# Kernel optimization log

Measured on AMD Instinct MI355X. Metric: run time of the kernel, lower is better.

Reference implementation:

```python
import jax, jax.numpy as jnp
import numpy as np

B, T, D, H = 32, 1024, 1024, 1024


def gru_cell(x, h, W_ih, W_hh, b_ih, b_hh):
    # torch.nn.GRUCell math; gate order (r, z, n)
    gi = x @ W_ih.T + b_ih          # [B, 3H]
    gh = h @ W_hh.T + b_hh          # [B, 3H]
    i_r, i_z, i_n = jnp.split(gi, 3, axis=-1)
    h_r, h_z, h_n = jnp.split(gh, 3, axis=-1)
    r = jax.nn.sigmoid(i_r + h_r)
    z = jax.nn.sigmoid(i_z + h_z)
    n = jnp.tanh(i_n + r * h_n)
    return (1.0 - z) * n + z * h


def setup_inputs() -> dict:
    key = jax.random.key(0)
    k = jax.random.split(key, 6)
    scale = np.float32(1.0 / np.sqrt(H))  # torch GRUCell init range
    x = jax.random.normal(k[0], (B, T, D), jnp.float32)
    seg = jax.random.randint(k[1], (B, T), 0, 2).astype(jnp.int32)
    W_ih = jax.random.normal(k[2], (3 * H, D), jnp.float32) * scale
    W_hh = jax.random.normal(k[3], (3 * H, H), jnp.float32) * scale
    b_ih = jax.random.normal(k[4], (3 * H,), jnp.float32) * scale
    b_hh = jax.random.normal(k[5], (3 * H,), jnp.float32) * scale
    return {"x": x, "W_ih": W_ih, "W_hh": W_hh, "b_ih": b_ih, "b_hh": b_hh, "seg": seg}


def reference(x, W_ih, W_hh, b_ih, b_hh, seg):
    # apply_rnn_pack: GRUCell scan with segment-masked reset + ragged pack.
    segf = seg.astype(x.dtype)

    def step(h, inp):
        xt, st = inp                      # xt [B,D], st [B]
        h_new = gru_cell(xt, h, W_ih, W_hh, b_ih, b_hh)
        h_next = st[:, None] * h_new      # reset hidden where seg==0
        return h_next, h_new              # emit pre-reset hidden

    h0 = jnp.zeros((B, H), x.dtype)
    xs = (jnp.swapaxes(x, 0, 1), jnp.swapaxes(segf, 0, 1))
    _, hs = jax.lax.scan(step, h0, xs)    # hs [T,B,H]
    hs = jnp.swapaxes(hs, 0, 1)           # [B,T,H]

    # Pack: write h at step t into slot (#emits before t) iff seg[b,t]==0.
    emit = seg == 0                       # [B,T]
    pos = jnp.cumsum(emit, axis=1) - 1    # destination slot for emitted steps
    pos = jnp.where(emit, pos, T)         # route non-emitted steps to pad slot
    out = jnp.zeros((B, T + 1, H), x.dtype)
    b_idx = jnp.arange(B)[:, None]
    out = out.at[b_idx, pos].set(hs)
    out = out[:, :T]                      # [B,T,H], ragged-padded with zeros
    counts = emit.sum(axis=1)             # per-sample packed lengths (idx)
    return out, counts
```

## Files before the change

kernel.cpp:

```cpp
#include <hip/hip_runtime.h>

#define NB 32
#define NT 1024
#define ND 1024
#define NH 1024
#define G3 3072
#define MROWS 32768
#define HROWS 16512
#define GSROWS 32896
#define TAILG 128

typedef __bf16 bf16x8 __attribute__((ext_vector_type(8)));
typedef float f32x4 __attribute__((ext_vector_type(4)));
typedef unsigned short u16x8 __attribute__((ext_vector_type(8)));
typedef unsigned short u16x4 __attribute__((ext_vector_type(4)));

__device__ __forceinline__ float b2f(unsigned short u){
  union { unsigned int i; float f; } v; v.i = ((unsigned int)u) << 16; return v.f;
}
__device__ __forceinline__ unsigned short f2b(float f){
  union { float f; unsigned int i; } v; v.f = f;
  unsigned int r = (v.i + 0x7FFFu + ((v.i >> 16) & 1u)) >> 16;
  return (unsigned short)r;
}
__device__ __forceinline__ float sigm(float x){ return 1.0f / (1.0f + __expf(-x)); }
__device__ __forceinline__ float tanh_(float x){ return 2.0f / (1.0f + __expf(-2.0f * x)) - 1.0f; }

__device__ __forceinline__ void g2l16(const void* g, void* l){
  __builtin_amdgcn_global_load_lds((__attribute__((address_space(1))) void*)g,
                                   (__attribute__((address_space(3))) void*)l, 16, 0, 0);
}

__global__ __launch_bounds__(256) void k_setup(const float* __restrict__ wih,
    const float* __restrict__ whh, const float* __restrict__ x,
    unsigned short* __restrict__ wih_b, unsigned short* __restrict__ whh_b,
    unsigned short* __restrict__ x_b, int has_xb, f32x4* __restrict__ outv, int out_n4){
  int i0 = blockIdx.x * 256 + threadIdx.x;
  int stride = gridDim.x * 256;
  f32x4 z = {0.f, 0.f, 0.f, 0.f};
  for (int j = i0; j < out_n4; j += stride) __builtin_nontemporal_store(z, &outv[j]);
  int nw4 = (G3 * ND) / 4;
  for (int j = i0; j < nw4; j += stride){
    f32x4 a = ((const f32x4*)wih)[j];
    f32x4 b = ((const f32x4*)whh)[j];
    u16x4 ua = {f2b(a[0]), f2b(a[1]), f2b(a[2]), f2b(a[3])};
    u16x4 ub = {f2b(b[0]), f2b(b[1]), f2b(b[2]), f2b(b[3])};
    ((u16x4*)wih_b)[j] = ua;
    ((u16x4*)whh_b)[j] = ub;
  }
  if (has_xb){
    int nx4 = (MROWS * ND) / 4;
    for (int j = i0; j < nx4; j += stride){
      f32x4 a = ((const f32x4*)x)[j];
      u16x4 u = {f2b(a[0]), f2b(a[1]), f2b(a[2]), f2b(a[3])};
      ((u16x4*)x_b)[j] = u;
    }
  }
}

__global__ __launch_bounds__(1024) void k_segbuild(const int* __restrict__ seg,
    int* __restrict__ ugi, int* __restrict__ uout, int* __restrict__ ulen,
    int* __restrict__ nseg_b,
    int* __restrict__ sgi, int* __restrict__ sout, int* __restrict__ slen,
    int* __restrict__ cnt_ge, int* __restrict__ base_g,
    unsigned int* __restrict__ perm, unsigned int* __restrict__ bar,
    float* __restrict__ counts_out){
  __shared__ int hist[1025];
  __shared__ int sufx[1024];
  __shared__ int pref[1024];
  __shared__ int offs[1025];
  int tid = threadIdx.x;
  int wave = tid >> 6, lane = tid & 63;
  if (tid == 0) *bar = 0u;

  for (int b = wave; b < NB; b += 16){
    int prev = -1;
    int zc = 0;
    for (int c = 0; c < 16; ++c){
      int t = c * 64 + lane;
      int v = seg[b * NT + t];
      unsigned long long mask = __ballot(v == 0);
      unsigned long long below = mask & ((1ULL << lane) - 1ULL);
      if (v == 0){
        int pz = below ? (c * 64 + (63 - __clzll((long long)below))) : prev;
        int eidx = zc + __popcll(below);
        int slot = b * NT + eidx;
        ugi[slot]  = b * NT + (pz + 1);
        uout[slot] = b * NT + eidx;
        ulen[slot] = t - pz;
      }
      if (mask) prev = c * 64 + (63 - __clzll((long long)mask));
      zc += __popcll(mask);
    }
    if (lane == 0){ nseg_b[b] = zc; counts_out[b] = (float)zc; }
  }
  __syncthreads();
  for (int i = tid; i <= 1024; i += 1024) hist[i] = 0;
  __syncthreads();
  for (int s = tid; s < NB * NT; s += 1024){
    int b = s >> 10, j = s & 1023;
    if (j < nseg_b[b]) atomicAdd(&hist[ulen[s]], 1);
  }
  __syncthreads();
  if (tid < 1024) sufx[tid] = hist[tid + 1];
  __syncthreads();
  for (int off = 1; off < 1024; off <<= 1){
    int v = (tid + off < 1024) ? sufx[tid + off] : 0;
    __syncthreads();
    sufx[tid] += v;
    __syncthreads();
  }
  cnt_ge[tid + 1] = sufx[tid];
  if (tid == 0){ cnt_ge[0] = sufx[0]; cnt_ge[1025] = 0; }
  offs[tid] = sufx[tid];
  if (tid == 0) offs[1024] = 0;
  pref[tid] = sufx[tid];
  __syncthreads();
  for (int off = 1; off < 1024; off <<= 1){
    int v = (tid >= off) ? pref[tid - off] : 0;
    __syncthreads();
    pref[tid] += v;
    __syncthreads();
  }
  base_g[tid + 1] = pref[tid];
  if (tid == 0){ base_g[0] = 0; base_g[1025] = pref[1023]; }
  __syncthreads();
  for (int s = tid; s < NB * NT; s += 1024){
    int b = s >> 10, j = s & 1023;
    if (j < nseg_b[b]){
      int len = ulen[s];
      int p = atomicAdd(&offs[len], 1);
      sgi[p] = ugi[s]; sout[p] = uout[s]; slen[p] = len;
    }
  }
  for (int m = tid; m < MROWS; m += 1024) perm[m] = 0xFFFFFFFFu;
  __syncthreads();
  int nseg = cnt_ge[1];
  for (int p = tid; p < nseg; p += 1024){
    int src = sgi[p];
    int len = slen[p];
    perm[src] = (unsigned int)p;
    for (int kk = 1; kk < len; ++kk)
      perm[src + kk] = (unsigned int)(pref[kk - 1] + p);
  }
}

__global__ __launch_bounds__(256, 2) void k_gi_gemm(const float* __restrict__ x,
    const unsigned short* __restrict__ x_b, const unsigned short* __restrict__ wih_b,
    const float* __restrict__ b_ih, const unsigned int* __restrict__ perm,
    unsigned short* __restrict__ gs, int use_xb){
  __shared__ unsigned short Alds[128 * 64];
  __shared__ unsigned short Blds[128 * 64];
  int tid = threadIdx.x;
  int w = tid >> 6, lane = tid & 63;
  int mtile = blockIdx.x / 24, ntile = blockIdx.x % 24;
  int m0 = mtile * 128, n0 = ntile * 128;
  int mh = (w >> 1) * 64, nh = (w & 1) * 64;
  int lrow = lane >> 3;
  int lcol = 8 * ((lane & 7) ^ lrow);
  f32x4 acc[4][4];
#pragma unroll
  for (int i = 0; i < 4; ++i)
#pragma unroll
    for (int j = 0; j < 4; ++j) acc[i][j] = (f32x4){0.f, 0.f, 0.f, 0.f};

  for (int kc = 0; kc < 16; ++kc){
    __syncthreads();
    if (use_xb){
#pragma unroll
      for (int p = 0; p < 4; ++p){
        int s = w * 4 + p;
        g2l16(x_b + (size_t)(m0 + s * 8 + lrow) * ND + kc * 64 + lcol, &Alds[s * 512]);
      }
    } else {
#pragma unroll
      for (int p = 0; p < 4; ++p){
        int e = (p * 256 + tid) * 8;
        int r = e >> 6, c = e & 63;
        const float* src = x + (size_t)(m0 + r) * ND + kc * 64 + c;
        f32x4 f0 = *(const f32x4*)src;
        f32x4 f1 = *(const f32x4*)(src + 4);
        u16x8 u;
        u[0]=f2b(f0[0]); u[1]=f2b(f0[1]); u[2]=f2b(f0[2]); u[3]=f2b(f0[3]);
        u[4]=f2b(f1[0]); u[5]=f2b(f1[1]); u[6]=f2b(f1[2]); u[7]=f2b(f1[3]);
        *(u16x8*)&Alds[r * 64 + (c ^ ((r & 7) << 3))] = u;
      }
    }
#pragma unroll
    for (int p = 0; p < 4; ++p){
      int s = w * 4 + p;
      g2l16(wih_b + (size_t)(n0 + s * 8 + lrow) * ND + kc * 64 + lcol, &Blds[s * 512]);
    }
    __syncthreads();
#pragma unroll
    for (int ks = 0; ks < 2; ++ks){
      int co = ks * 32 + (lane >> 4) * 8;
      int cx = co ^ ((lane & 7) << 3);
      bf16x8 a[4], bb[4];
#pragma unroll
      for (int mi = 0; mi < 4; ++mi)
        a[mi] = *(const bf16x8*)&Alds[(mh + mi * 16 + (lane & 15)) * 64 + cx];
#pragma unroll
      for (int ni = 0; ni < 4; ++ni)
        bb[ni] = *(const bf16x8*)&Blds[(nh + ni * 16 + (lane & 15)) * 64 + cx];
#pragma unroll
      for (int mi = 0; mi < 4; ++mi)
#pragma unroll
        for (int ni = 0; ni < 4; ++ni)
          acc[mi][ni] = __builtin_amdgcn_mfma_f32_16x16x32_bf16(a[mi], bb[ni], acc[mi][ni], 0, 0, 0);
    }
  }
#pragma unroll
  for (int mi = 0; mi < 4; ++mi){
    int rbase = m0 + mh + mi * 16 + (lane >> 4) * 4;
#pragma unroll
    for (int rr = 0; rr < 4; ++rr){
      unsigned int prow = perm[rbase + rr];
      if (prow == 0xFFFFFFFFu) continue;
#pragma unroll
      for (int ni = 0; ni < 4; ++ni){
        int col = n0 + nh + ni * 16 + (lane & 15);
        __builtin_nontemporal_store(f2b(acc[mi][ni][rr] + b_ih[col]),
                                    &gs[(size_t)prow * G3 + col]);
      }
    }
  }
}

__global__ __launch_bounds__(256) void k_step0(const float* __restrict__ b_hh,
    const unsigned short* __restrict__ gs,
    const int* __restrict__ sout, const int* __restrict__ cnt_ge,
    unsigned short* __restrict__ hbuf, float* __restrict__ out){
  int nseg = cnt_ge[1];
  int c2 = cnt_ge[2];
  int total = nseg * 128;
  for (int idx = blockIdx.x * 256 + threadIdx.x; idx < total; idx += gridDim.x * 256){
    int i = idx >> 7;
    int c0 = (idx & 127) * 8;
    bool emit = (i >= c2);
    const unsigned short* g = gs + (size_t)i * G3;
    u16x8 vr = __builtin_nontemporal_load((const u16x8*)(g + c0));
    u16x8 vz = __builtin_nontemporal_load((const u16x8*)(g + NH + c0));
    u16x8 vn = __builtin_nontemporal_load((const u16x8*)(g + 2 * NH + c0));
    float hn[8];
#pragma unroll
    for (int j = 0; j < 8; ++j){
      int c = c0 + j;
      float r = sigm(b2f(vr[j]) + b_hh[c]);
      float z = sigm(b2f(vz[j]) + b_hh[NH + c]);
      float n = tanh_(b2f(vn[j]) + r * b_hh[2 * NH + c]);
      hn[j] = (1.0f - z) * n;
    }
    if (emit){
      float* orow = out + (size_t)sout[i] * NH + c0;
      f32x4 v0 = {hn[0], hn[1], hn[2], hn[3]};
      f32x4 v1 = {hn[4], hn[5], hn[6], hn[7]};
      __builtin_nontemporal_store(v0, (f32x4*)orow);
      __builtin_nontemporal_store(v1, (f32x4*)(orow + 4));
    } else {
      u16x8 u;
#pragma unroll
      for (int j = 0; j < 8; ++j) u[j] = f2b(hn[j]);
      *(u16x8*)(hbuf + (size_t)HROWS * NH + (size_t)i * NH + c0) = u;
    }
  }
}

__device__ __forceinline__ void step_tile(int m0, int nc0, int Ak, int c2, int gbase,
    const unsigned short* __restrict__ whh_b, const float* __restrict__ b_hh,
    const unsigned short* __restrict__ gs, const int* __restrict__ sout,
    const unsigned short* __restrict__ hread, unsigned short* __restrict__ hwrite,
    float* __restrict__ out,
    unsigned short (*Alds)[64 * 128], unsigned short (*Blds)[192 * 128]){
  int tid = threadIdx.x;
  int w = tid >> 6, lane = tid & 63;
  int l15 = lane & 15, l4 = lane >> 4;

#define STAGE2(buf, kc) do {                                                        \
    _Pragma("unroll")                                                               \
    for (int p = 0; p < 4; ++p){                                                    \
      int s = w * 4 + p;                                                            \
      int ar = s * 4 + l4;                                                          \
      int sc = (l15 * 8) ^ ((ar & 7) << 3);                                         \
      g2l16(hread + (size_t)(m0 + ar) * NH + (kc) * 128 + sc, &Alds[buf][s * 512]); \
    }                                                                               \
    _Pragma("unroll")                                                               \
    for (int p = 0; p < 12; ++p){                                                   \
      int s = w * 12 + p;                                                           \
      int br = s * 4 + l4;                                                          \
      int wrow = (br >> 6) * NH + nc0 + (br & 63);                                  \
      int sc = (l15 * 8) ^ ((br & 7) << 3);                                         \
      g2l16(whh_b + (size_t)wrow * NH + (kc) * 128 + sc, &Blds[buf][s * 512]);      \
    }                                                                               \
  } while (0)

  STAGE2(0, 0);

  int c_lane = nc0 + w * 16 + l15;
  float bh_r = b_hh[c_lane], bh_z = b_hh[NH + c_lane], bh_n = b_hh[2 * NH + c_lane];
  unsigned short gr_[4][4], gz_[4][4], gn_[4][4], hv_[4][4];
  int so_[4][4];
#pragma unroll
  for (int a = 0; a < 4; ++a){
#pragma unroll
    for (int rr = 0; rr < 4; ++rr){
      int i = m0 + a * 16 + l4 * 4 + rr;
      const unsigned short* g = gs + (size_t)(gbase + i) * G3 + c_lane;
      gr_[a][rr] = __builtin_nontemporal_load(g);
      gz_[a][rr] = __builtin_nontemporal_load(g + NH);
      gn_[a][rr] = __builtin_nontemporal_load(g + 2 * NH);
      hv_[a][rr] = hread[(size_t)i * NH + c_lane];
      so_[a][rr] = sout[i < MROWS ? i : 0];
    }
  }

  f32x4 acc[4][3];
#pragma unroll
  for (int a = 0; a < 4; ++a)
#pragma unroll
    for (int b = 0; b < 3; ++b) acc[a][b] = (f32x4){0.f, 0.f, 0.f, 0.f};

  __syncthreads();
  int cur = 0;
  for (int kc = 0; kc < 8; ++kc){
    if (kc < 7) STAGE2(cur ^ 1, kc + 1);
#pragma unroll
    for (int ks = 0; ks < 4; ++ks){
      int co = ks * 32 + l4 * 8;
      bf16x8 av[4], bv[3];
#pragma unroll
      for (int a = 0; a < 4; ++a){
        int r = a * 16 + l15;
        av[a] = *(const bf16x8*)&Alds[cur][r * 128 + (co ^ ((r & 7) << 3))];
      }
#pragma unroll
      for (int b = 0; b < 3; ++b){
        int br = 64 * b + w * 16 + l15;
        bv[b] = *(const bf16x8*)&Blds[cur][br * 128 + (co ^ ((br & 7) << 3))];
      }
#pragma unroll
      for (int a = 0; a < 4; ++a)
#pragma unroll
        for (int b = 0; b < 3; ++b)
          acc[a][b] = __builtin_amdgcn_mfma_f32_16x16x32_bf16(av[a], bv[b], acc[a][b], 0, 0, 0);
    }
    __syncthreads();
    cur ^= 1;
  }
#undef STAGE2

#pragma unroll
  for (int a = 0; a < 4; ++a){
#pragma unroll
    for (int rr = 0; rr < 4; ++rr){
      int i = m0 + a * 16 + l4 * 4 + rr;
      if (i >= Ak) continue;
      bool emit = (i >= c2);
      float ghr = acc[a][0][rr] + bh_r;
      float ghz = acc[a][1][rr] + bh_z;
      float ghn = acc[a][2][rr] + bh_n;
      float h = b2f(hv_[a][rr]);
      float r = sigm(b2f(gr_[a][rr]) + ghr);
      float z = sigm(b2f(gz_[a][rr]) + ghz);
      float n = tanh_(b2f(gn_[a][rr]) + r * ghn);
      float hn = (1.0f - z) * n + z * h;
      if (emit) __builtin_nontemporal_store(hn, &out[(size_t)so_[a][rr] * NH + c_lane]);
      else      hwrite[(size_t)i * NH + c_lane] = f2b(hn);
    }
  }
}

__global__ __launch_bounds__(256, 1) void k_step(int k,
    const unsigned short* __restrict__ whh_b, const float* __restrict__ b_hh,
    const unsigned short* __restrict__ gs, const int* __restrict__ base_g,
    const int* __restrict__ sout, const int* __restrict__ cnt_ge,
    unsigned short* __restrict__ hbuf, float* __restrict__ out){
  __shared__ unsigned short Alds[2][64 * 128];
  __shared__ unsigned short Blds[2][192 * 128];
  int Ak = cnt_ge[k + 1];
  if (Ak <= 0) return;
  int c2 = cnt_ge[k + 2];
  int gbase = base_g[k];
  int Mt = (Ak + 63) >> 6;
  int tiles = Mt * 16;
  const unsigned short* hread = hbuf + (size_t)(k & 1) * HROWS * NH;
  unsigned short* hwrite      = hbuf + (size_t)((k + 1) & 1) * HROWS * NH;
  for (int t = blockIdx.x; t < tiles; t += gridDim.x){
    int cs = t & 15, mt = t >> 4;
    step_tile(mt * 64, cs * 64, Ak, c2, gbase, whh_b, b_hh, gs, sout,
              hread, hwrite, out, Alds, Blds);
  }
}

__global__ __launch_bounds__(256, 1) void k_tail(
    const unsigned short* __restrict__ whh_b, const float* __restrict__ b_hh,
    const unsigned short* __restrict__ gs, const int* __restrict__ base_g,
    const int* __restrict__ sout, const int* __restrict__ cnt_ge,
    unsigned short* __restrict__ hbuf, float* __restrict__ out,
    unsigned int* __restrict__ bar){
  __shared__ unsigned short Alds[2][64 * 128];
  __shared__ unsigned short Blds[2][192 * 128];
  unsigned int phase = 0;
  for (int k = 5; k <= 1023; ++k){
    int Ak = cnt_ge[k + 1];
    if (Ak <= 0) break;
    int c2 = cnt_ge[k + 2];
    int gbase = base_g[k];
    int Mt = (Ak + 63) >> 6;
    int tiles = Mt * 16;
    const unsigned short* hread = hbuf + (size_t)(k & 1) * HROWS * NH;
    unsigned short* hwrite      = hbuf + (size_t)((k + 1) & 1) * HROWS * NH;
    for (int t = blockIdx.x; t < tiles; t += TAILG){
      int cs = t & 15, mt = t >> 4;
      step_tile(mt * 64, cs * 64, Ak, c2, gbase, whh_b, b_hh, gs, sout,
                hread, hwrite, out, Alds, Blds);
    }
    ++phase;
    __syncthreads();
    if (threadIdx.x == 0){
      __threadfence();
      atomicAdd(bar, 1u);
      unsigned int goal = phase * (unsigned int)TAILG;
      while (__hip_atomic_load(bar, __ATOMIC_RELAXED, __HIP_MEMORY_SCOPE_AGENT) < goal)
        __builtin_amdgcn_s_sleep(4);
      __threadfence();
    }
    __syncthreads();
  }
}

extern "C" void kernel_launch(void* const* d_in, const int* in_sizes, int n_in,
                              void* d_out, int out_size, void* d_ws, size_t ws_size,
                              hipStream_t stream){
  (void)in_sizes; (void)n_in;
  const float* x   = (const float*)d_in[0];
  const float* wih = (const float*)d_in[1];
  const float* whh = (const float*)d_in[2];
  const float* bih = (const float*)d_in[3];
  const float* bhh = (const float*)d_in[4];
  const int*   seg = (const int*)d_in[5];
  float* outp = (float*)d_out;

  char* ws = (char*)d_ws;
  size_t o_wih = 0;
  size_t o_whh = 6291456;
  size_t o_gs  = 12582912;
  size_t o_desc = o_gs + (size_t)GSROWS * G3 * 2;
  size_t o_h    = o_desc + (2u << 20);
  size_t o_xb   = o_h + (size_t)2 * HROWS * NH * 2;
  size_t need_xb = o_xb + (size_t)MROWS * ND * 2;
  int has_xb = (ws_size >= need_xb) ? 1 : 0;

  unsigned short* wih_b = (unsigned short*)(ws + o_wih);
  unsigned short* whh_b = (unsigned short*)(ws + o_whh);
  unsigned short* gsort = (unsigned short*)(ws + o_gs);
  int* ugi  = (int*)(ws + o_desc);
  int* uout = ugi + 32768;
  int* ulen = uout + 32768;
  int* sgi  = ulen + 32768;
  int* sout = sgi + 32768;
  int* slen = sout + 32768;
  int* nsegb = slen + 32768;
  int* cntge = nsegb + 64;
  int* baseg = cntge + 1056;
  unsigned int* perm = (unsigned int*)(baseg + 1056);
  unsigned int* bar  = perm + MROWS;
  unsigned short* hbuf = (unsigned short*)(ws + o_h);
  unsigned short* x_b  = (unsigned short*)(ws + o_xb);

  float* counts_out = outp + (size_t)NB * NT * NH;
  int out_n4 = out_size / 4;

  k_setup<<<dim3(4096), dim3(256), 0, stream>>>(wih, whh, x, wih_b, whh_b, x_b, has_xb,
                                                (f32x4*)d_out, out_n4);

  k_segbuild<<<dim3(1), dim3(1024), 0, stream>>>(seg, ugi, uout, ulen, nsegb,
                                                 sgi, sout, slen, cntge, baseg,
                                                 perm, bar, counts_out);

  k_gi_gemm<<<dim3(256 * 24), dim3(256), 0, stream>>>(x, x_b, wih_b, bih, perm, gsort, has_xb);

  k_step0<<<dim3(1024), dim3(256), 0, stream>>>(bhh, gsort, sout, cntge, hbuf, outp);

  static const int grids[5] = {0, 1024, 1024, 512, 256};
  for (int k = 1; k <= 4; ++k){
    k_step<<<dim3(grids[k]), dim3(256), 0, stream>>>(k, whh_b, bhh, gsort, baseg,
                                                     sout, cntge, hbuf, outp);
  }

  k_tail<<<dim3(TAILG), dim3(256), 0, stream>>>(whh_b, bhh, gsort, baseg,
                                                sout, cntge, hbuf, outp, bar);
}
```

Baseline: 1.038 ms.

## Use per-wave 16x16 MFMA tiles in tail kernel with more persistent blocks

In the tail phase, the LDS-staged 64x192 block tile is replaced with per-wave 16-row by 16-column units. Each unit computes all three gates with direct global bf16 loads and MFMA 16x16x32, then applies the GRU epilogue in registers. Persistent blocks double to 256 with two blocks per CU, so the shrinking active batch in late steps is split across many more waves. The cost is losing LDS reuse of A and B operands, which raises global and L2 traffic, and the grid barrier now has more participants.

```diff
diff --git a/kernel.cpp b/kernel.cpp
--- a/kernel.cpp
+++ b/kernel.cpp
@@ -8,7 +8,7 @@
 #define MROWS 32768
 #define HROWS 16512
 #define GSROWS 32896
-#define TAILG 128
+#define TAILG 256
 
 typedef __bf16 bf16x8 __attribute__((ext_vector_type(8)));
 typedef float f32x4 __attribute__((ext_vector_type(4)));
@@ -392,29 +392,78 @@
   }
 }
 
-__global__ __launch_bounds__(256, 1) void k_tail(
+__global__ __launch_bounds__(256, 2) void k_tail(
     const unsigned short* __restrict__ whh_b, const float* __restrict__ b_hh,
     const unsigned short* __restrict__ gs, const int* __restrict__ base_g,
     const int* __restrict__ sout, const int* __restrict__ cnt_ge,
     unsigned short* __restrict__ hbuf, float* __restrict__ out,
     unsigned int* __restrict__ bar){
-  __shared__ unsigned short Alds[2][64 * 128];
-  __shared__ unsigned short Blds[2][192 * 128];
+  int tid = threadIdx.x;
+  int w = tid >> 6, lane = tid & 63;
+  int l15 = lane & 15, l4 = lane >> 4;
+  int gwave = blockIdx.x * 4 + w;
+  const int NWAVES = TAILG * 4;
   unsigned int phase = 0;
   for (int k = 5; k <= 1023; ++k){
     int Ak = cnt_ge[k + 1];
     if (Ak <= 0) break;
     int c2 = cnt_ge[k + 2];
     int gbase = base_g[k];
-    int Mt = (Ak + 63) >> 6;
-    int tiles = Mt * 16;
+    int Mt = (Ak + 15) >> 4;
+    int units = Mt * 64;
     const unsigned short* hread = hbuf + (size_t)(k & 1) * HROWS * NH;
     unsigned short* hwrite      = hbuf + (size_t)((k + 1) & 1) * HROWS * NH;
-    for (int t = blockIdx.x; t < tiles; t += TAILG){
-      int cs = t & 15, mt = t >> 4;
-      step_tile(mt * 64, cs * 64, Ak, c2, gbase, whh_b, b_hh, gs, sout,
-                hread, hwrite, out, Alds, Blds);
-    }
+
+    for (int u = gwave; u < units; u += NWAVES){
+      int cs = u & 63, mt = u >> 6;
+      int m0 = mt * 16;
+      int c_lane = cs * 16 + l15;
+
+      float bh_r = b_hh[c_lane], bh_z = b_hh[NH + c_lane], bh_n = b_hh[2 * NH + c_lane];
+      unsigned short gr_[4], gz_[4], gn_[4], hv_[4];
+      int so_[4];
+#pragma unroll
+      for (int rr = 0; rr < 4; ++rr){
+        int i = m0 + l4 * 4 + rr;
+        const unsigned short* g = gs + (size_t)(gbase + i) * G3 + c_lane;
+        gr_[rr] = __builtin_nontemporal_load(g);
+        gz_[rr] = __builtin_nontemporal_load(g + NH);
+        gn_[rr] = __builtin_nontemporal_load(g + 2 * NH);
+        hv_[rr] = hread[(size_t)i * NH + c_lane];
+        so_[rr] = sout[i < MROWS ? i : 0];
+      }
+
+      const unsigned short* arow  = hread + (size_t)(m0 + l15) * NH + l4 * 8;
+      const unsigned short* brow0 = whh_b + (size_t)(0 * NH + cs * 16 + l15) * NH + l4 * 8;
+      const unsigned short* brow1 = whh_b + (size_t)(1 * NH + cs * 16 + l15) * NH + l4 * 8;
+      const unsigned short* brow2 = whh_b + (size_t)(2 * NH + cs * 16 + l15) * NH + l4 * 8;
+      f32x4 acc0 = {0.f, 0.f, 0.f, 0.f}, acc1 = acc0, acc2 = acc0;
+#pragma unroll 4
+      for (int ks = 0; ks < 32; ++ks){
+        bf16x8 a  = *(const bf16x8*)(arow  + ks * 32);
+        bf16x8 b0 = *(const bf16x8*)(brow0 + ks * 32);
+        bf16x8 b1 = *(const bf16x8*)(brow1 + ks * 32);
+        bf16x8 b2 = *(const bf16x8*)(brow2 + ks * 32);
+        acc0 = __builtin_amdgcn_mfma_f32_16x16x32_bf16(a, b0, acc0, 0, 0, 0);
+        acc1 = __builtin_amdgcn_mfma_f32_16x16x32_bf16(a, b1, acc1, 0, 0, 0);
+        acc2 = __builtin_amdgcn_mfma_f32_16x16x32_bf16(a, b2, acc2, 0, 0, 0);
+      }
+
+#pragma unroll
+      for (int rr = 0; rr < 4; ++rr){
+        int i = m0 + l4 * 4 + rr;
+        if (i >= Ak) continue;
+        bool emit = (i >= c2);
+        float h = b2f(hv_[rr]);
+        float r = sigm(b2f(gr_[rr]) + acc0[rr] + bh_r);
+        float z = sigm(b2f(gz_[rr]) + acc1[rr] + bh_z);
+        float n = tanh_(b2f(gn_[rr]) + r * (acc2[rr] + bh_n));
+        float hn = (1.0f - z) * n + z * h;
+        if (emit) __builtin_nontemporal_store(hn, &out[(size_t)so_[rr] * NH + c_lane]);
+        else      hwrite[(size_t)i * NH + c_lane] = f2b(hn);
+      }
+    }
+
     ++phase;
     __syncthreads();
     if (threadIdx.x == 0){
```

After: 1.249 ms. 1.2x slower.
